# Optimization experiments

Measured on AMD Instinct MI355X. Metric: run time of the kernel, lower is better.

Reference implementation:

```python
import math
import jax, jax.numpy as jnp
import numpy as np

HEADS = 16


def setup_inputs() -> dict:
    key = jax.random.key(0)
    k1, k2, k3, k4, k5 = jax.random.split(key, 5)
    B, S, D = 2, 2048, 1024
    return {
        "x": jax.random.normal(k1, (B, S, D), dtype=jnp.float32),
        "Wqkv": jax.random.normal(k2, (3 * D, D), dtype=jnp.float32) * (1.0 / math.sqrt(D)),
        "bqkv": jax.random.normal(k3, (3 * D,), dtype=jnp.float32) * 0.02,
        "Wo": jax.random.normal(k4, (D, D), dtype=jnp.float32) * (1.0 / math.sqrt(D)),
        "bo": jax.random.normal(k5, (D,), dtype=jnp.float32) * 0.02,
    }


def reference(x, Wqkv, bqkv, Wo, bo):
    B, S, D = x.shape
    H = HEADS
    hd = D // H  # head dim
    qkv = x @ Wqkv.T + bqkv                      # (B, S, 3D)
    # Faithful to torch: direct contiguous reshape (NOT a transpose-based head split)
    qkv = qkv.reshape(B, H, S, 3 * hd)           # (B, H, S, 3*hd)
    q, k, v = jnp.split(qkv, 3, axis=-1)         # each (B, H, S, hd)
    scores = jnp.einsum("bhsd,bhtd->bhst", q, k) * (1.0 / math.sqrt(hd))
    attn = jax.nn.softmax(scores, axis=-1)       # (B, H, S, S)
    vals = jnp.einsum("bhst,bhtd->bhsd", attn, v)
    vals = vals.reshape(B, S, D)                 # faithful direct reshape back
    return vals @ Wo.T + bo
```

## Files before the change

### kernel.cpp

```cpp
#include <hip/hip_runtime.h>
#include <stdint.h>

typedef unsigned short u16;
typedef __attribute__((ext_vector_type(8))) short short8;
typedef __attribute__((ext_vector_type(4))) float f32x4;
typedef __attribute__((ext_vector_type(16))) float f32x16;
typedef __attribute__((ext_vector_type(8))) __bf16 bf16x8;
typedef __attribute__((ext_vector_type(4))) unsigned u32x4;

#define DEV static __device__ __forceinline__

template <typename T>
DEV auto mfma_try(T a, T b, f32x4 c, int)
    -> decltype(__builtin_amdgcn_mfma_f32_16x16x32_bf16(a, b, c, 0, 0, 0)) {
  return __builtin_amdgcn_mfma_f32_16x16x32_bf16(a, b, c, 0, 0, 0);
}
template <typename T>
DEV f32x4 mfma_try(T a, T b, f32x4 c, long) {
  return __builtin_amdgcn_mfma_f32_16x16x32_bf16(
      __builtin_bit_cast(bf16x8, a), __builtin_bit_cast(bf16x8, b), c, 0, 0, 0);
}
DEV f32x4 MFMA(short8 a, short8 b, f32x4 c) { return mfma_try(a, b, c, 0); }

template <typename T>
DEV auto mfma32_try(T a, T b, f32x16 c, int)
    -> decltype(__builtin_amdgcn_mfma_f32_32x32x16_bf16(a, b, c, 0, 0, 0)) {
  return __builtin_amdgcn_mfma_f32_32x32x16_bf16(a, b, c, 0, 0, 0);
}
template <typename T>
DEV f32x16 mfma32_try(T a, T b, f32x16 c, long) {
  return __builtin_amdgcn_mfma_f32_32x32x16_bf16(
      __builtin_bit_cast(bf16x8, a), __builtin_bit_cast(bf16x8, b), c, 0, 0, 0);
}
DEV f32x16 MFMA32(short8 a, short8 b, f32x16 c) { return mfma32_try(a, b, c, 0); }

DEV void gload16(const u16* g, u16* lds) {
  __builtin_amdgcn_global_load_lds((unsigned int*)g, (unsigned int*)lds, 16, 0, 0);
}

DEV u16 f2bf(float f) {
  unsigned u = __float_as_uint(f);
  u = (u + 0x7FFFu + ((u >> 16) & 1u)) >> 16;
  return (u16)u;
}

DEV float exp2fast(float x) {
  float r;
  asm("v_exp_f32 %0, %1" : "=v"(r) : "v"(x));
  return r;
}

DEV unsigned cvtpk_bf16(float lo, float hi_) {
  unsigned r;
  asm("v_cvt_pk_bf16_f32 %0, %1, %2" : "=v"(r) : "v"(lo), "v"(hi_));
  return r;
}

DEV void permswap(unsigned& a, unsigned& b) {
  asm volatile("v_permlane32_swap_b32 %0, %1" : "+v"(a), "+v"(b));
}

__global__ void cvt_kernel(const float* __restrict__ x, const float* __restrict__ wq,
                           const float* __restrict__ wo, u16* __restrict__ xb,
                           u16* __restrict__ wqb, u16* __restrict__ wob) {
  const int N1 = 4194304 / 4, N2 = 3145728 / 4, N3 = 1048576 / 4;
  const int total = N1 + N2 + N3;
  for (int i = blockIdx.x * blockDim.x + threadIdx.x; i < total;
       i += gridDim.x * blockDim.x) {
    const float4* s;
    u16* d;
    int off;
    if (i < N1) { s = (const float4*)x; d = xb; off = i; }
    else if (i < N1 + N2) { s = (const float4*)wq; d = wqb; off = i - N1; }
    else { s = (const float4*)wo; d = wob; off = i - N1 - N2; }
    float4 v = s[off];
    ushort4 o;
    o.x = f2bf(v.x); o.y = f2bf(v.y); o.z = f2bf(v.z); o.w = f2bf(v.w);
    ((ushort4*)d)[off] = o;
  }
}

__global__ __launch_bounds__(512, 2) void gemm1_256(
    const u16* __restrict__ A, const u16* __restrict__ Bm,
    const float* __restrict__ bias,
    u16* __restrict__ Qb, u16* __restrict__ Kb, u16* __restrict__ Vb) {
  extern __shared__ __align__(16) u16 SM[];
  const int K = 1024;
  const int tid = threadIdx.x;
  const int lane = tid & 63;
  const int wave = tid >> 6;
  const int wr = wave >> 2;
  const int wc = wave & 3;
  const int l15 = lane & 15, l4 = lane >> 4;

  const int bid = blockIdx.x;
  const int wg = (bid & 7) * 32 + (bid >> 3);
  const int by = wg >> 4, bx = wg & 15;
  const int m0 = by * 256, n0 = bx * 192;

  f32x4 acc[8][3] = {};

  const int srr = tid >> 3, scb = tid & 7;
  const int ssw = (scb ^ (srr & 7)) * 8;

  auto panel = [&](int Tn, int q) {
    const u16* src =
        (q < 4) ? A + (size_t)(m0 + q * 64 + srr) * K + Tn * 64 + ssw
                : Bm + (size_t)(n0 + (q - 4) * 64 + srr) * K + Tn * 64 + ssw;
    gload16(src, SM + ((Tn & 1) * 7 + q) * 4096 + tid * 8);
  };

#pragma unroll
  for (int q = 0; q < 7; ++q) panel(0, q);

  for (int T = 0; T < 16; ++T) {
    const int base = (T & 1) * 7;
    short8 bf[3];
#pragma unroll
    for (int p = 0; p < 4; ++p) {
      if (T + 1 < 16) {
        if (p == 0) { panel(T + 1, 0); panel(T + 1, 2); }
        else if (p == 1) { panel(T + 1, 1); panel(T + 1, 3); }
        else if (p == 2) { panel(T + 1, 4); panel(T + 1, 5); }
        else { panel(T + 1, 6); }
      }
      if (p == 0) {
        if (T + 1 < 16) asm volatile("s_waitcnt vmcnt(2)" ::: "memory");
        else asm volatile("s_waitcnt vmcnt(0)" ::: "memory");
      }
      __builtin_amdgcn_s_barrier();

      const int g = p & 1, kk = p >> 1;
      if (g == 0) {
#pragma unroll
        for (int nj = 0; nj < 3; ++nj) {
          const int rb = wc * 48 + nj * 16 + l15;
          const int qb = 4 + (rb >> 6), rrb = rb & 63;
          bf[nj] = *(const short8*)(SM + (base + qb) * 4096 + rrb * 64 +
                                    (((kk * 4 + l4) ^ (rrb & 7)) * 8));
        }
      }
      short8 af[4];
      const int qa = wr * 2 + g;
#pragma unroll
      for (int mi = 0; mi < 4; ++mi) {
        const int rr = mi * 16 + l15;
        af[mi] = *(const short8*)(SM + (base + qa) * 4096 + rr * 64 +
                                  (((kk * 4 + l4) ^ (rr & 7)) * 8));
      }
      __builtin_amdgcn_s_setprio(1);
#pragma unroll
      for (int mi = 0; mi < 4; ++mi)
#pragma unroll
        for (int nj = 0; nj < 3; ++nj)
          acc[g * 4 + mi][nj] = MFMA(af[mi], bf[nj], acc[g * 4 + mi][nj]);
      __builtin_amdgcn_s_setprio(0);
    }
  }
  __syncthreads();

#pragma unroll
  for (int nj = 0; nj < 3; ++nj) {
    const int cl = wc * 48 + nj * 16 + l15;
    const float bv = bias[n0 + cl];
#pragma unroll
    for (int mi = 0; mi < 8; ++mi)
#pragma unroll
      for (int r = 0; r < 4; ++r) {
        const int ml = wr * 128 + mi * 16 + l4 * 4 + r;
        SM[ml * 200 + cl] = f2bf(acc[mi][nj][r] + bv);
      }
  }
  __syncthreads();

  for (int k = tid; k < 768; k += 512) {
    const int ml = k & 255, h = k >> 8;
    const int m = m0 + ml;
    const int s = m & 2047;
    const int bh = (m >> 11) * 16 + (s >> 7);
    const int s2 = (s & 127) * 16 + bx;
    u16* const dst = (h == 0) ? Qb : ((h == 1) ? Kb : Vb);
    u16* const drow = dst + ((size_t)bh * 2048 + s2) * 64;
    const u16* const srow = SM + ml * 200 + h * 64;
#pragma unroll
    for (int g2 = 0; g2 < 8; ++g2)
      *(short8*)(drow + g2 * 8) = *(const short8*)(srow + g2 * 8);
  }
}

__global__ __launch_bounds__(256, 4) void gemm2_64(
    const u16* __restrict__ A, const u16* __restrict__ Bm,
    const float* __restrict__ bias, float* __restrict__ Cf) {
  __shared__ u16 SM2[2 * 6144];
  const int K = 1024, N = 1024;
  const int tid = threadIdx.x;
  const int lane = tid & 63;
  const int wave = tid >> 6;
  const int l15 = lane & 15, l4 = lane >> 4;
  const int m0 = blockIdx.y * 64, n0 = blockIdx.x * 128;

  f32x4 acc[4][2] = {};

  const u16* ga = A + (size_t)(m0 + (tid >> 2)) * K + (tid & 3) * 8;
  const u16* gb = Bm + (size_t)(n0 + (tid >> 2)) * K + (tid & 3) * 8;
  const size_t rstep = (size_t)64 * K;

  auto stage = [&](int buf, int kt) {
    u16* la = SM2 + buf * 6144 + tid * 8;
    u16* lb = SM2 + buf * 6144 + 2048 + tid * 8;
    gload16(ga + kt, la);
    gload16(gb + kt, lb);
    gload16(gb + kt + rstep, lb + 2048);
  };

  stage(0, 0);
  for (int t = 0; t < 32; ++t) {
    const int cur = t & 1;
    if (t + 1 < 32) {
      stage(cur ^ 1, (t + 1) * 32);
      asm volatile("s_waitcnt vmcnt(3)" ::: "memory");
    } else {
      asm volatile("s_waitcnt vmcnt(0)" ::: "memory");
    }
    __builtin_amdgcn_s_barrier();

    const u16* As = SM2 + cur * 6144;
    const u16* Bs = As + 2048;
    short8 af[4], bfr[2];
#pragma unroll
    for (int i = 0; i < 4; ++i)
      af[i] = *(const short8*)(As + (i * 16 + l15) * 32 + l4 * 8);
#pragma unroll
    for (int j = 0; j < 2; ++j)
      bfr[j] = *(const short8*)(Bs + (wave * 32 + j * 16 + l15) * 32 + l4 * 8);
    __builtin_amdgcn_s_setprio(1);
#pragma unroll
    for (int i = 0; i < 4; ++i)
#pragma unroll
      for (int j = 0; j < 2; ++j) acc[i][j] = MFMA(af[i], bfr[j], acc[i][j]);
    __builtin_amdgcn_s_setprio(0);
    __builtin_amdgcn_s_barrier();
  }

#pragma unroll
  for (int nj = 0; nj < 2; ++nj) {
    const int c = n0 + wave * 32 + nj * 16 + l15;
    const float bv = bias[c];
#pragma unroll
    for (int mi = 0; mi < 4; ++mi)
#pragma unroll
      for (int r = 0; r < 4; ++r) {
        const int m = m0 + mi * 16 + l4 * 4 + r;
        Cf[(size_t)m * N + c] = acc[mi][nj][r] + bv;
      }
  }
}

__global__ __launch_bounds__(256) void vtrans_kernel(const u16* __restrict__ Vn,
                                                     u16* __restrict__ VT) {
  __shared__ u16 T[64 * 72];
  const int tid = threadIdx.x;
  const int bh = blockIdx.x >> 5;
  const int s0 = (blockIdx.x & 31) * 64;
  const int r = tid >> 3, c8 = tid & 7;
#pragma unroll
  for (int i = 0; i < 2; ++i) {
    const int s = r + i * 32;
    short8 v = *(const short8*)(Vn + ((size_t)bh * 2048 + s0 + s) * 64 + c8 * 8);
#pragma unroll
    for (int j = 0; j < 8; ++j) T[(c8 * 8 + j) * 72 + s] = (u16)v[j];
  }
  __syncthreads();
#pragma unroll
  for (int i = 0; i < 2; ++i) {
    const int d = (tid >> 3) + i * 32;
    short8 v = *(const short8*)(&T[d * 72 + (tid & 7) * 8]);
    *(short8*)(VT + ((size_t)bh * 64 + d) * 2048 + s0 + (tid & 7) * 8) = v;
  }
}

__global__ __launch_bounds__(512) void attn_kernel(
    const u16* __restrict__ Qg, const u16* __restrict__ Kg,
    const u16* __restrict__ VTg, u16* __restrict__ v2) {
  __shared__ __align__(16) char smem[65536];
  u16* const KS = (u16*)smem;
  u16* const VS = (u16*)smem + 16384;
  float* const FM = (float*)smem;

  const int tid = threadIdx.x;
  const int lane = tid & 63;
  const int half = tid >> 8;
  const int tid256 = tid & 255;
  const int w4 = (tid >> 6) & 3;
  const int l31 = lane & 31;
  const int hi = lane >> 5;

  const int bid = blockIdx.x;
  const int logical = (bid & 7) * 64 + (bid >> 3);
  const int bh = logical >> 4;
  const int qt = logical & 15;

  const u16* Qh = Qg + (size_t)bh * 2048 * 64;
  const u16* Kh = Kg + (size_t)bh * 2048 * 64;
  const u16* VTh = VTg + (size_t)bh * 64 * 2048;

  const int q0 = qt * 128 + w4 * 32;
  const float C1 = 0.18033688f;

  short8 qf[4];
#pragma unroll
  for (int d_ = 0; d_ < 4; ++d_)
    qf[d_] = *(const short8*)(Qh + (size_t)(q0 + l31) * 64 + d_ * 16 + hi * 8);

  f32x16 ot[2] = {};
  float ls4[4] = {0.f, 0.f, 0.f, 0.f};

  const int r8 = tid256 >> 3;
  const int c16 = tid256 & 7;
  const int xr = l31 & 7;
  const int Tbase = half * 16;

  auto stage = [&](int buf, int T) {
    u16* kd = KS + (half * 2 + buf) * 4096 + tid256 * 8;
    u16* vd = VS + (half * 2 + buf) * 4096 + tid256 * 8;
#pragma unroll
    for (int i = 0; i < 2; ++i) {
      const int row = i * 32 + r8;
      gload16(Kh + (size_t)(T * 64 + row) * 64 + ((c16 ^ (row & 7)) * 8),
              kd + i * 2048);
    }
#pragma unroll
    for (int i = 0; i < 2; ++i) {
      const int d = i * 32 + r8;
      gload16(VTh + (size_t)d * 2048 + T * 64 + ((c16 ^ (d & 7)) * 8),
              vd + i * 2048);
    }
  };

  stage(0, Tbase);
  __syncthreads();

  for (int t = 0; t < 16; ++t) {
    const int cur = t & 1;
    if (t + 1 < 16) stage(cur ^ 1, Tbase + t + 1);

    const u16* Kb = KS + (half * 2 + cur) * 4096;
    const u16* Vb = VS + (half * 2 + cur) * 4096;

    f32x16 st[2] = {};
    __builtin_amdgcn_s_setprio(1);
#pragma unroll
    for (int n = 0; n < 2; ++n)
#pragma unroll
      for (int d_ = 0; d_ < 4; ++d_) {
        short8 kf = *(const short8*)(Kb + (n * 32 + l31) * 64 +
                                     (((d_ * 2 + hi) ^ xr) * 8));
        st[n] = MFMA32(kf, qf[d_], st[n]);
      }
    __builtin_amdgcn_s_setprio(0);

#pragma unroll
    for (int r = 0; r < 16; ++r) {
      st[0][r] = exp2fast(st[0][r] * C1);
      st[1][r] = exp2fast(st[1][r] * C1);
    }
#pragma unroll
    for (int i = 0; i < 4; ++i)
      ls4[i] += ((st[0][i] + st[0][i + 4]) + (st[0][i + 8] + st[0][i + 12])) +
                ((st[1][i] + st[1][i + 4]) + (st[1][i + 8] + st[1][i + 12]));

    short8 pf[2][2];
#pragma unroll
    for (int n = 0; n < 2; ++n) {
      unsigned W[4][2];
#pragma unroll
      for (int j = 0; j < 4; ++j)
#pragma unroll
        for (int pp = 0; pp < 2; ++pp)
          W[j][pp] = cvtpk_bf16(st[n][4 * j + 2 * pp], st[n][4 * j + 2 * pp + 1]);
#pragma unroll
      for (int ks = 0; ks < 2; ++ks) {
        unsigned x0 = W[2 * ks][0], y0 = W[2 * ks + 1][0];
        unsigned x1 = W[2 * ks][1], y1 = W[2 * ks + 1][1];
        permswap(x0, y0);
        permswap(x1, y1);
        u32x4 pw = {x0, x1, y0, y1};
        pf[n][ks] = __builtin_bit_cast(short8, pw);
      }
    }

    __builtin_amdgcn_s_setprio(1);
#pragma unroll
    for (int db = 0; db < 2; ++db)
#pragma unroll
      for (int ksg = 0; ksg < 4; ++ksg) {
        short8 vf = *(const short8*)(Vb + (db * 32 + l31) * 64 +
                                     (((ksg * 2 + hi) ^ xr) * 8));
        ot[db] = MFMA32(vf, pf[ksg >> 1][ksg & 1], ot[db]);
      }
    __builtin_amdgcn_s_setprio(0);

    __syncthreads();
  }

  float l = (ls4[0] + ls4[1]) + (ls4[2] + ls4[3]);
  l += __shfl_xor(l, 32);

  if (half == 1) {
    float* F = FM + (size_t)(w4 * 64 + lane) * 33;
#pragma unroll
    for (int r = 0; r < 16; ++r) {
      F[r] = ot[0][r];
      F[16 + r] = ot[1][r];
    }
    F[32] = l;
  }
  __syncthreads();
  if (half == 0) {
    const float* F = FM + (size_t)(w4 * 64 + lane) * 33;
    const float inv = 1.0f / (l + F[32]);

    const int s2v = q0 + l31;
    const int rowO = (bh >> 4) * 2048 + (bh & 15) * 128 + (s2v >> 4);
    const int colb = (s2v & 15) * 64;
#pragma unroll
    for (int db = 0; db < 2; ++db)
#pragma unroll
      for (int g = 0; g < 4; ++g) {
        ushort4 w;
        w.x = f2bf((ot[db][4 * g + 0] + F[db * 16 + 4 * g + 0]) * inv);
        w.y = f2bf((ot[db][4 * g + 1] + F[db * 16 + 4 * g + 1]) * inv);
        w.z = f2bf((ot[db][4 * g + 2] + F[db * 16 + 4 * g + 2]) * inv);
        w.w = f2bf((ot[db][4 * g + 3] + F[db * 16 + 4 * g + 3]) * inv);
        const int d = db * 32 + 8 * g + 4 * hi;
        *(ushort4*)(v2 + (size_t)rowO * 1024 + colb + d) = w;
      }
  }
}

extern "C" void kernel_launch(void* const* d_in, const int* in_sizes, int n_in,
                              void* d_out, int out_size, void* d_ws, size_t ws_size,
                              hipStream_t stream) {
  const float* x = (const float*)d_in[0];
  const float* Wqkv = (const float*)d_in[1];
  const float* bqkv = (const float*)d_in[2];
  const float* Wo = (const float*)d_in[3];
  const float* bo = (const float*)d_in[4];
  float* out = (float*)d_out;

  char* ws = (char*)d_ws;
  u16* xb   = (u16*)(ws);
  u16* wqb  = (u16*)(ws + 8388608);
  u16* wob  = (u16*)(ws + 14680064);
  u16* Qb   = (u16*)(ws + 16777216);
  u16* Kb   = (u16*)(ws + 25165824);
  u16* VTb  = (u16*)(ws + 33554432);
  u16* v2   = (u16*)(ws + 41943040);
  u16* Vnat = v2;

  cvt_kernel<<<2048, 256, 0, stream>>>(x, Wqkv, Wo, xb, wqb, wob);

  hipFuncSetAttribute((const void*)gemm1_256,
                      hipFuncAttributeMaxDynamicSharedMemorySize, 114688);
  gemm1_256<<<256, 512, 114688, stream>>>(xb, wqb, bqkv, Qb, Kb, Vnat);

  vtrans_kernel<<<1024, 256, 0, stream>>>(Vnat, VTb);

  attn_kernel<<<512, 512, 0, stream>>>(Qb, Kb, VTb, v2);

  dim3 g2(8, 64);
  gemm2_64<<<g2, 256, 0, stream>>>(v2, wob, bo, out);
}
```

Measured before the change: 111.3 us.

## Switch QKV GEMM to 256x256 tiles with half-panel staged pipeline

```diff
diff --git a/kernel.cpp b/kernel.cpp
--- a/kernel.cpp
+++ b/kernel.cpp
@@ -80,7 +80,7 @@
   }
 }
 
-__global__ __launch_bounds__(512, 2) void gemm1_256(
+__global__ __launch_bounds__(512) void gemm1_256ph(
     const u16* __restrict__ A, const u16* __restrict__ Bm,
     const float* __restrict__ bias,
     u16* __restrict__ Qb, u16* __restrict__ Kb, u16* __restrict__ Vb) {
@@ -94,94 +94,101 @@
   const int l15 = lane & 15, l4 = lane >> 4;
 
   const int bid = blockIdx.x;
-  const int wg = (bid & 7) * 32 + (bid >> 3);
-  const int by = wg >> 4, bx = wg & 15;
-  const int m0 = by * 256, n0 = bx * 192;
-
-  f32x4 acc[8][3] = {};
-
-  const int srr = tid >> 3, scb = tid & 7;
-  const int ssw = (scb ^ (srr & 7)) * 8;
-
-  auto panel = [&](int Tn, int q) {
-    const u16* src =
-        (q < 4) ? A + (size_t)(m0 + q * 64 + srr) * K + Tn * 64 + ssw
-                : Bm + (size_t)(n0 + (q - 4) * 64 + srr) * K + Tn * 64 + ssw;
-    gload16(src, SM + ((Tn & 1) * 7 + q) * 4096 + tid * 8);
+  const int wg = (bid & 7) * 24 + (bid >> 3);
+  const int by = wg / 12, bx = wg - (wg / 12) * 12;
+  const int m0 = by * 256, n0 = bx * 256;
+
+  f32x4 acc[8][4] = {};
+
+  auto stageHalf = [&](int T, int op, int half) {
+#pragma unroll
+    for (int i = 0; i < 2; ++i) {
+      const int idx = i * 512 + tid;
+      const int r = idx >> 3, cb = idx & 7;
+      const u16* src =
+          (op == 0)
+              ? A + (size_t)(m0 + half * 128 + r) * K + T * 64 + ((cb ^ (r & 7)) * 8)
+              : Bm + (size_t)(n0 + half * 128 + r) * K + T * 64 + ((cb ^ (r & 7)) * 8);
+      gload16(src, SM + (T & 1) * 32768 + op * 16384 + half * 8192 + idx * 8);
+    }
   };
 
-#pragma unroll
-  for (int q = 0; q < 7; ++q) panel(0, q);
+  stageHalf(0, 0, 0);
+  stageHalf(0, 0, 1);
+  stageHalf(0, 1, 0);
+  stageHalf(0, 1, 1);
+
+  const int bhalf = wc >> 1;
+  const int brow0 = (wc & 1) * 64;
 
   for (int T = 0; T < 16; ++T) {
-    const int base = (T & 1) * 7;
-    short8 bf[3];
+    const int base = (T & 1) * 32768;
+    asm volatile("s_waitcnt vmcnt(0)" ::: "memory");
+    __builtin_amdgcn_s_barrier();
+
+    short8 bf[4][2];
+#pragma unroll
+    for (int nj = 0; nj < 4; ++nj)
+#pragma unroll
+      for (int kk = 0; kk < 2; ++kk) {
+        const int rr = brow0 + nj * 16 + l15;
+        bf[nj][kk] = *(const short8*)(SM + base + 16384 + bhalf * 8192 + rr * 64 +
+                                      (((kk * 4 + l4) ^ (rr & 7)) * 8));
+      }
+
 #pragma unroll
     for (int p = 0; p < 4; ++p) {
-      if (T + 1 < 16) {
-        if (p == 0) { panel(T + 1, 0); panel(T + 1, 2); }
-        else if (p == 1) { panel(T + 1, 1); panel(T + 1, 3); }
-        else if (p == 2) { panel(T + 1, 4); panel(T + 1, 5); }
-        else { panel(T + 1, 6); }
-      }
-      if (p == 0) {
-        if (T + 1 < 16) asm volatile("s_waitcnt vmcnt(2)" ::: "memory");
-        else asm volatile("s_waitcnt vmcnt(0)" ::: "memory");
-      }
-      __builtin_amdgcn_s_barrier();
-
-      const int g = p & 1, kk = p >> 1;
-      if (g == 0) {
-#pragma unroll
-        for (int nj = 0; nj < 3; ++nj) {
-          const int rb = wc * 48 + nj * 16 + l15;
-          const int qb = 4 + (rb >> 6), rrb = rb & 63;
-          bf[nj] = *(const short8*)(SM + (base + qb) * 4096 + rrb * 64 +
-                                    (((kk * 4 + l4) ^ (rrb & 7)) * 8));
+      if (T + 1 < 16) stageHalf(T + 1, p >> 1, p & 1);
+      short8 af[2][2];
+#pragma unroll
+      for (int m2 = 0; m2 < 2; ++m2)
+#pragma unroll
+        for (int kk = 0; kk < 2; ++kk) {
+          const int rr = (p * 2 + m2) * 16 + l15;
+          af[m2][kk] = *(const short8*)(SM + base + wr * 8192 + rr * 64 +
+                                        (((kk * 4 + l4) ^ (rr & 7)) * 8));
         }
-      }
-      short8 af[4];
-      const int qa = wr * 2 + g;
-#pragma unroll
-      for (int mi = 0; mi < 4; ++mi) {
-        const int rr = mi * 16 + l15;
-        af[mi] = *(const short8*)(SM + (base + qa) * 4096 + rr * 64 +
-                                  (((kk * 4 + l4) ^ (rr & 7)) * 8));
-      }
       __builtin_amdgcn_s_setprio(1);
 #pragma unroll
-      for (int mi = 0; mi < 4; ++mi)
-#pragma unroll
-        for (int nj = 0; nj < 3; ++nj)
-          acc[g * 4 + mi][nj] = MFMA(af[mi], bf[nj], acc[g * 4 + mi][nj]);
+      for (int m2 = 0; m2 < 2; ++m2)
+#pragma unroll
+        for (int nj = 0; nj < 4; ++nj)
+#pragma unroll
+          for (int kk = 0; kk < 2; ++kk)
+            acc[p * 2 + m2][nj] = MFMA(af[m2][kk], bf[nj][kk], acc[p * 2 + m2][nj]);
       __builtin_amdgcn_s_setprio(0);
     }
   }
+
+  asm volatile("s_waitcnt vmcnt(0)" ::: "memory");
   __syncthreads();
 
 #pragma unroll
-  for (int nj = 0; nj < 3; ++nj) {
-    const int cl = wc * 48 + nj * 16 + l15;
+  for (int nj = 0; nj < 4; ++nj) {
+    const int cl = wc * 64 + nj * 16 + l15;
     const float bv = bias[n0 + cl];
 #pragma unroll
     for (int mi = 0; mi < 8; ++mi)
 #pragma unroll
       for (int r = 0; r < 4; ++r) {
         const int ml = wr * 128 + mi * 16 + l4 * 4 + r;
-        SM[ml * 200 + cl] = f2bf(acc[mi][nj][r] + bv);
+        SM[ml * 264 + cl] = f2bf(acc[mi][nj][r] + bv);
       }
   }
   __syncthreads();
 
-  for (int k = tid; k < 768; k += 512) {
+  for (int k = tid; k < 1024; k += 512) {
     const int ml = k & 255, h = k >> 8;
     const int m = m0 + ml;
+    const int c0 = n0 + h * 64;
+    const int chunk = c0 / 192;
+    const int sel = (c0 - chunk * 192) >> 6;
+    u16* const dst = (sel == 0) ? Qb : ((sel == 1) ? Kb : Vb);
     const int s = m & 2047;
     const int bh = (m >> 11) * 16 + (s >> 7);
-    const int s2 = (s & 127) * 16 + bx;
-    u16* const dst = (h == 0) ? Qb : ((h == 1) ? Kb : Vb);
+    const int s2 = (s & 127) * 16 + chunk;
     u16* const drow = dst + ((size_t)bh * 2048 + s2) * 64;
-    const u16* const srow = SM + ml * 200 + h * 64;
+    const u16* const srow = SM + ml * 264 + h * 64;
 #pragma unroll
     for (int g2 = 0; g2 < 8; ++g2)
       *(short8*)(drow + g2 * 8) = *(const short8*)(srow + g2 * 8);
@@ -460,9 +467,9 @@
 
   cvt_kernel<<<2048, 256, 0, stream>>>(x, Wqkv, Wo, xb, wqb, wob);
 
-  hipFuncSetAttribute((const void*)gemm1_256,
-                      hipFuncAttributeMaxDynamicSharedMemorySize, 114688);
-  gemm1_256<<<256, 512, 114688, stream>>>(xb, wqb, bqkv, Qb, Kb, Vnat);
+  hipFuncSetAttribute((const void*)gemm1_256ph,
+                      hipFuncAttributeMaxDynamicSharedMemorySize, 139264);
+  gemm1_256ph<<<192, 512, 139264, stream>>>(xb, wqb, bqkv, Qb, Kb, Vnat);
 
   vtrans_kernel<<<1024, 256, 0, stream>>>(Vnat, VTb);
 
```

Measured after the change: 115.1 us. 3.4% more time.

## Restructure QKV GEMM to triple-buffered K=32 stages with two-ahead prefetch

Applied to the files above, without the earlier changes.

```diff
diff --git a/kernel.cpp b/kernel.cpp
--- a/kernel.cpp
+++ b/kernel.cpp
@@ -80,7 +80,7 @@
   }
 }
 
-__global__ __launch_bounds__(512, 2) void gemm1_256(
+__global__ __launch_bounds__(512) void gemm1_256r(
     const u16* __restrict__ A, const u16* __restrict__ Bm,
     const float* __restrict__ bias,
     u16* __restrict__ Qb, u16* __restrict__ Kb, u16* __restrict__ Vb) {
@@ -100,63 +100,92 @@
 
   f32x4 acc[8][3] = {};
 
-  const int srr = tid >> 3, scb = tid & 7;
-  const int ssw = (scb ^ (srr & 7)) * 8;
-
-  auto panel = [&](int Tn, int q) {
+  auto stagePair = [&](int T, int qa_, int qb_) {
+    const int q = (tid < 256) ? qa_ : qb_;
+    const int b = tid & 255;
+    const int r = b >> 2, cb = b & 3;
     const u16* src =
-        (q < 4) ? A + (size_t)(m0 + q * 64 + srr) * K + Tn * 64 + ssw
-                : Bm + (size_t)(n0 + (q - 4) * 64 + srr) * K + Tn * 64 + ssw;
-    gload16(src, SM + ((Tn & 1) * 7 + q) * 4096 + tid * 8);
+        (q < 4) ? A + (size_t)(m0 + q * 64 + r) * K + T * 32 + ((cb ^ (r & 3)) * 8)
+                : Bm + (size_t)(n0 + (q - 4) * 64 + r) * K + T * 32 +
+                      ((cb ^ (r & 3)) * 8);
+    gload16(src, SM + ((T % 3) * 7 + q) * 2048 + b * 8);
   };
-
-#pragma unroll
-  for (int q = 0; q < 7; ++q) panel(0, q);
-
-  for (int T = 0; T < 16; ++T) {
-    const int base = (T & 1) * 7;
+  auto stageSingle = [&](int T, int q) {
+    if (tid < 256) {
+      const int b = tid;
+      const int r = b >> 2, cb = b & 3;
+      const u16* src = Bm + (size_t)(n0 + (q - 4) * 64 + r) * K + T * 32 +
+                       ((cb ^ (r & 3)) * 8);
+      gload16(src, SM + ((T % 3) * 7 + q) * 2048 + b * 8);
+    }
+  };
+
+#pragma unroll
+  for (int t = 0; t < 2; ++t) {
+    stagePair(t, 0, 1);
+    stagePair(t, 2, 3);
+    stagePair(t, 4, 5);
+    stageSingle(t, 6);
+  }
+
+  for (int T = 0; T < 32; ++T) {
+    if (T < 30) asm volatile("s_waitcnt vmcnt(3)" ::: "memory");
+    else asm volatile("s_waitcnt vmcnt(0)" ::: "memory");
+    __builtin_amdgcn_s_barrier();
+
+    const int base = (T % 3) * 7;
+
+    if (T + 2 < 32) {
+      stagePair(T + 2, 0, 1);
+      stagePair(T + 2, 2, 3);
+    }
     short8 bf[3];
 #pragma unroll
-    for (int p = 0; p < 4; ++p) {
-      if (T + 1 < 16) {
-        if (p == 0) { panel(T + 1, 0); panel(T + 1, 2); }
-        else if (p == 1) { panel(T + 1, 1); panel(T + 1, 3); }
-        else if (p == 2) { panel(T + 1, 4); panel(T + 1, 5); }
-        else { panel(T + 1, 6); }
-      }
-      if (p == 0) {
-        if (T + 1 < 16) asm volatile("s_waitcnt vmcnt(2)" ::: "memory");
-        else asm volatile("s_waitcnt vmcnt(0)" ::: "memory");
-      }
-      __builtin_amdgcn_s_barrier();
-
-      const int g = p & 1, kk = p >> 1;
-      if (g == 0) {
-#pragma unroll
-        for (int nj = 0; nj < 3; ++nj) {
-          const int rb = wc * 48 + nj * 16 + l15;
-          const int qb = 4 + (rb >> 6), rrb = rb & 63;
-          bf[nj] = *(const short8*)(SM + (base + qb) * 4096 + rrb * 64 +
-                                    (((kk * 4 + l4) ^ (rrb & 7)) * 8));
-        }
-      }
+    for (int nj = 0; nj < 3; ++nj) {
+      const int rb = wc * 48 + nj * 16 + l15;
+      const int pb = rb >> 6, rrb = rb & 63;
+      bf[nj] = *(const short8*)(SM + (base + 4 + pb) * 2048 + rrb * 32 +
+                                ((l4 ^ (rrb & 3)) * 8));
+    }
+    {
       short8 af[4];
-      const int qa = wr * 2 + g;
 #pragma unroll
       for (int mi = 0; mi < 4; ++mi) {
-        const int rr = mi * 16 + l15;
-        af[mi] = *(const short8*)(SM + (base + qa) * 4096 + rr * 64 +
-                                  (((kk * 4 + l4) ^ (rr & 7)) * 8));
+        const int rra = mi * 16 + l15;
+        af[mi] = *(const short8*)(SM + (base + wr * 2) * 2048 + rra * 32 +
+                                  ((l4 ^ (rra & 3)) * 8));
       }
       __builtin_amdgcn_s_setprio(1);
 #pragma unroll
       for (int mi = 0; mi < 4; ++mi)
 #pragma unroll
         for (int nj = 0; nj < 3; ++nj)
-          acc[g * 4 + mi][nj] = MFMA(af[mi], bf[nj], acc[g * 4 + mi][nj]);
+          acc[mi][nj] = MFMA(af[mi], bf[nj], acc[mi][nj]);
       __builtin_amdgcn_s_setprio(0);
     }
-  }
+
+    if (T + 2 < 32) {
+      stagePair(T + 2, 4, 5);
+      stageSingle(T + 2, 6);
+    }
+    {
+      short8 af[4];
+#pragma unroll
+      for (int mi = 0; mi < 4; ++mi) {
+        const int rra = mi * 16 + l15;
+        af[mi] = *(const short8*)(SM + (base + wr * 2 + 1) * 2048 + rra * 32 +
+                                  ((l4 ^ (rra & 3)) * 8));
+      }
+      __builtin_amdgcn_s_setprio(1);
+#pragma unroll
+      for (int mi = 0; mi < 4; ++mi)
+#pragma unroll
+        for (int nj = 0; nj < 3; ++nj)
+          acc[4 + mi][nj] = MFMA(af[mi], bf[nj], acc[4 + mi][nj]);
+      __builtin_amdgcn_s_setprio(0);
+    }
+  }
+
   __syncthreads();
 
 #pragma unroll
@@ -460,9 +489,9 @@
 
   cvt_kernel<<<2048, 256, 0, stream>>>(x, Wqkv, Wo, xb, wqb, wob);
 
-  hipFuncSetAttribute((const void*)gemm1_256,
-                      hipFuncAttributeMaxDynamicSharedMemorySize, 114688);
-  gemm1_256<<<256, 512, 114688, stream>>>(xb, wqb, bqkv, Qb, Kb, Vnat);
+  hipFuncSetAttribute((const void*)gemm1_256r,
+                      hipFuncAttributeMaxDynamicSharedMemorySize, 102400);
+  gemm1_256r<<<256, 512, 102400, stream>>>(xb, wqb, bqkv, Qb, Kb, Vnat);
 
   vtrans_kernel<<<1024, 256, 0, stream>>>(Vnat, VTb);
 
```

Result: slower. 114.7 us (+3.1%).
